# Performance work log

Measured on AMD Instinct MI355X. Metric: run time of the kernel, lower is better.

The kernel has to match this reference:

```python
import jax, jax.numpy as jnp
import numpy as np

N_U = 20000; N_I = 20000; D = 256
NNZ = 600000; EGG = 300000; EDD = 300000; B = 8192
DROP = 0.1; LAM2 = 1e-7


def _attention(x, W, a, edges):
    # GAT-style attention over sampled relationship edges (src -> tgt).
    n, d = x.shape
    h = x @ W                                  # [n, d]
    src, tgt = edges[0], edges[1]
    e = jax.nn.leaky_relu((h @ a[:d])[src] + (h @ a[d:])[tgt], 0.2)  # [E]
    m = jax.ops.segment_max(e, tgt, num_segments=n)
    m = jnp.where(jnp.isfinite(m), m, 0.0)
    ex = jnp.exp(e - m[tgt])
    denom = jax.ops.segment_sum(ex, tgt, num_segments=n)             # [n]
    num = jax.ops.segment_sum(ex[:, None] * h[src], tgt, num_segments=n)  # [n, d]
    return num / (denom[:, None] + 1e-9)


def _spmm(rows, cols, vals, x, n_out):
    # sparse [n_out, n_in] @ dense [n_in, d]
    return jax.ops.segment_sum(vals[:, None] * x[cols], rows, num_segments=n_out)


def _mlp(x, W1, b1, W2, b2, W3, b3):
    h = jax.nn.relu(x @ W1 + b1)
    h = jax.nn.relu(h @ W2 + b2)
    return (h @ W3 + b3)[..., 0]


def setup_inputs() -> dict:
    key = jax.random.key(0)
    ks = jax.random.split(key, 24)
    s = 0.02
    inp = {
        'E_g_0': jax.random.normal(ks[0], (N_U, D), jnp.float32) * s,
        'E_d_0': jax.random.normal(ks[1], (N_I, D), jnp.float32) * s,
        'att_W': jax.random.normal(ks[2], (D, D), jnp.float32) * s,
        'att_a': jax.random.normal(ks[3], (2 * D,), jnp.float32) * s,
        'att1_W': jax.random.normal(ks[4], (D, D), jnp.float32) * s,
        'att1_a': jax.random.normal(ks[5], (2 * D,), jnp.float32) * s,
        'W1': jax.random.normal(ks[6], (2 * D, D), jnp.float32) * s,
        'b1': jnp.zeros((D,), jnp.float32),
        'W2': jax.random.normal(ks[7], (D, D), jnp.float32) * s,
        'b2': jnp.zeros((D,), jnp.float32),
        'W3': jax.random.normal(ks[8], (D, 1), jnp.float32) * s,
        'b3': jnp.zeros((1,), jnp.float32),
        'M1': jax.random.normal(ks[9], (2 * D, D), jnp.float32) * s,
        'mb1': jnp.zeros((D,), jnp.float32),
        'M2': jax.random.normal(ks[10], (D, D), jnp.float32) * s,
        'mb2': jnp.zeros((D,), jnp.float32),
        'adj_vals': jax.random.uniform(ks[11], (NNZ,), jnp.float32),
        'uids': jax.random.randint(ks[12], (B,), 0, N_U, jnp.int32),
        'iids': jax.random.randint(ks[13], (B,), 0, N_I, jnp.int32),
        'pos': jax.random.randint(ks[14], (B,), 0, N_I, jnp.int32),
        'neg': jax.random.randint(ks[15], (B,), 0, N_I, jnp.int32),
        'gene_edges': jax.random.randint(ks[16], (2, EGG), 0, N_U, jnp.int32),
        'drug_edges': jax.random.randint(ks[17], (2, EDD), 0, N_I, jnp.int32),
        'adj_rows': jax.random.randint(ks[18], (NNZ,), 0, N_U, jnp.int32),
        'adj_cols': jax.random.randint(ks[19], (NNZ,), 0, N_I, jnp.int32),
        'drop1': jax.random.bernoulli(ks[20], 1.0 - DROP, (NNZ,)),
        'drop2': jax.random.bernoulli(ks[21], 1.0 - DROP, (NNZ,)),
    }
    return inp


def reference(E_g_0, E_d_0, att_W, att_a, att1_W, att1_a, W1, b1, W2, b2, W3, b3,
              M1, mb1, M2, mb2, adj_vals, uids, iids, pos, neg,
              gene_edges, drug_edges, adj_rows, adj_cols, drop1, drop2):
    # Attention-modulated layer-0 embeddings
    E_d0 = 0.1 * _attention(E_d_0, att_W, att_a, drug_edges) + E_d_0
    E_g0 = 0.1 * _attention(E_g_0, att_W, att_a, gene_edges) + E_g_0

    # sparse_dropout + spmm (two independent dropout draws, as in the source)
    scale = 1.0 / (1.0 - DROP)
    v1 = adj_vals * drop1.astype(adj_vals.dtype) * scale
    v2 = adj_vals * drop2.astype(adj_vals.dtype) * scale
    E_g = _spmm(adj_rows, adj_cols, v1, E_d0, N_U)   # adj @ E_d0
    E_d = _spmm(adj_cols, adj_rows, v2, E_g0, N_I)   # adj.T @ E_g0

    u = E_g[uids]; p = E_d[pos]; ng = E_d[neg]
    pos_s = _mlp(jnp.concatenate([u, p], axis=-1), W1, b1, W2, b2, W3, b3)
    neg_s = _mlp(jnp.concatenate([u, ng], axis=-1), W1, b1, W2, b2, W3, b3)

    # BCE-with-logits (labels 1 for pos, 0 for neg) + BPR term
    loss_pos = jnp.mean(jax.nn.softplus(-pos_s))
    loss_neg = jnp.mean(jax.nn.softplus(neg_s))
    loss_bpr = jnp.mean(jax.nn.softplus(-(pos_s - neg_s)))
    loss_r = loss_pos + loss_neg + loss_bpr

    params = (E_g_0, E_d_0, att_W, att_a, att1_W, att1_a,
              W1, b1, W2, b2, W3, b3, M1, mb1, M2, mb2)
    loss_reg = LAM2 * sum(jnp.sum(p_ * p_) for p_ in params)

    loss = loss_reg + loss_r  # loss_s == 0
    return jnp.stack([loss, loss_r, jnp.zeros((), loss.dtype)])
```

## Files before the change

### kernel.cpp

```cpp
#include <hip/hip_runtime.h>
#include <math.h>

#define N_NODES 20000
#define D       256
#define NNZ     600000
#define NEDGE   300000
#define BATCH   8192
#define DROP_SCALE (1.0f/0.9f)
#define LAM2_F  1e-7f

#define M_PAD   20096
#define CSTRIDE 20032

#define C_ATT 56
#define C_ADJ 80

#define BINW 320
#define NBIN 63
#define TILE_E 2048
#define EPT 8
#define T_ATT ((NEDGE + TILE_E - 1) / TILE_E)
#define T_ADJ ((NNZ + TILE_E - 1) / TILE_E)
#define NBLK_P1 (2 * T_ATT + 2 * T_ADJ)
#define CAP_BIN_ATT 5376
#define CAP_BIN_ADJ 6144

#define FP8_SCALE 256.0f
#define VSCALE    58980.0f
#define INV_VSCALE (1.0f/58980.0f)

typedef unsigned short u16;
typedef unsigned char  u8;
typedef __attribute__((ext_vector_type(8))) short bf16x8;
typedef __attribute__((ext_vector_type(4))) float f32x4;
typedef __attribute__((ext_vector_type(2))) float f32x2;
typedef __attribute__((ext_vector_type(4))) u16   v4h;
typedef __attribute__((ext_vector_type(4))) unsigned v4u;

__device__ inline float wave_reduce(float v) {
    #pragma unroll
    for (int off = 32; off > 0; off >>= 1) v += __shfl_down(v, off, 64);
    return v;
}

__device__ inline float softplus_f(float x) {
    float r = log1pf(__expf(-fabsf(x)));
    return x > 0.f ? x + r : r;
}

__device__ inline u16 f2bf(float f) {
    unsigned u = __float_as_uint(f);
    unsigned r = u + 0x7fff + ((u >> 16) & 1);
    return (u16)(r >> 16);
}
__device__ inline float bf2f(u16 b) { return __uint_as_float(((unsigned)b) << 16); }

__device__ inline u16 f2h(float f) {
    _Float16 h = (_Float16)f;
    return __builtin_bit_cast(u16, h);
}
__device__ inline float h2f(u16 b) {
    return (float)__builtin_bit_cast(_Float16, b);
}

__device__ inline unsigned f32x4_to_fp8x4(float a, float b, float c, float d) {
    int r = 0;
    r = __builtin_amdgcn_cvt_pk_fp8_f32(a, b, r, false);
    r = __builtin_amdgcn_cvt_pk_fp8_f32(c, d, r, true);
    return (unsigned)r;
}
__device__ inline u8 f32_to_fp8(float a) {
    int r = __builtin_amdgcn_cvt_pk_fp8_f32(a, a, 0, false);
    return (u8)(r & 0xff);
}

__device__ inline void gld_lds16(const void* g, void* l) {
    __builtin_amdgcn_global_load_lds((const __attribute__((address_space(1))) void*)g,
                                     (__attribute__((address_space(3))) void*)l, 16, 0, 0);
}

__global__ __launch_bounds__(256) void init_kernel(const unsigned char* __restrict__ drop,
                                                   const int* __restrict__ uids, const int* __restrict__ pos,
                                                   const int* __restrict__ neg,
                                                   const float* __restrict__ att_W, const float* __restrict__ att_a,
                                                   float* __restrict__ wlv, float* __restrict__ wrv,
                                                   unsigned* __restrict__ bm2, unsigned* __restrict__ bm3,
                                                   unsigned int* __restrict__ flag) {
    if (blockIdx.x < 96) {
        int i = blockIdx.x * blockDim.x + threadIdx.x;
        if (i < BATCH) {
            int v = uids[i];
            atomicOr(&bm2[v >> 5], 1u << (v & 31));
        } else if (i < 2 * BATCH) {
            int v = pos[i - BATCH];
            atomicOr(&bm3[v >> 5], 1u << (v & 31));
        } else {
            int v = neg[i - 2 * BATCH];
            atomicOr(&bm3[v >> 5], 1u << (v & 31));
        }
    } else if (blockIdx.x == 96) {
        __shared__ int cnt_s;
        if (threadIdx.x == 0) cnt_s = 0;
        __syncthreads();
        int c = 0;
        for (int i = threadIdx.x; i < 1024; i += blockDim.x)
            if (drop[4*i + 1] != 0) c++;
        atomicAdd(&cnt_s, c);
        __syncthreads();
        if (threadIdx.x == 0) *flag = (cnt_s > 64) ? 1u : 0u;
    } else {
        int t = threadIdx.x;
        float s1 = 0.f, s2 = 0.f;
        for (int n = 0; n < D; n++) {
            float w = att_W[(size_t)t * D + n];
            s1 += w * att_a[n];
            s2 += w * att_a[D + n];
        }
        wlv[t] = s1; wrv[t] = s2;
    }
}

#define NB_CAST (2 * M_PAD / 4)
#define NB_T1   (D * D / 256)
#define NB_T2   (2 * D * D / 256)
#define NB_T3   (D * D / 256)
#define NB_PREP (NB_CAST + NB_T1 + NB_T2 + NB_T3)
__global__ __launch_bounds__(256) void p1prep_kernel(
        const int* __restrict__ dtgt, const int* __restrict__ dsrc,
        const int* __restrict__ gtgt, const int* __restrict__ gsrc,
        const int* __restrict__ ar,   const int* __restrict__ ac,
        const float* __restrict__ vals,
        const void* __restrict__ drop1, const void* __restrict__ drop2,
        const unsigned int* __restrict__ flag,
        const unsigned* __restrict__ bm2, const unsigned* __restrict__ bm3,
        int* __restrict__ pcur, unsigned* __restrict__ attbin, uint2* __restrict__ adjbin,
        const float* __restrict__ E_g, const float* __restrict__ E_d,
        u16* __restrict__ Eg_bf, u16* __restrict__ Ed_bf,
        const float* __restrict__ att_W,
        const float* __restrict__ W1, const float* __restrict__ W2,
        u16* __restrict__ attWT, u16* __restrict__ W1T, u16* __restrict__ W2T,
        const float* __restrict__ wlv, const float* __restrict__ wrv,
        float* __restrict__ hl_g, float* __restrict__ hr_g,
        float* __restrict__ hl_d, float* __restrict__ hr_d,
        float* __restrict__ regp) {
    if (blockIdx.x < NBLK_P1) {
        __shared__ int hist[NBIN];
        __shared__ int basep[NBIN];
        for (int i = threadIdx.x; i < NBIN; i += 256) hist[i] = 0;
        __syncthreads();

        int b = blockIdx.x;
        int s, t0;
        if (b < T_ATT)               { s = 0; t0 = b; }
        else if (b < 2 * T_ATT)      { s = 1; t0 = b - T_ATT; }
        else if (b < 2*T_ATT + T_ADJ){ s = 2; t0 = b - 2 * T_ATT; }
        else                         { s = 3; t0 = b - 2 * T_ATT - T_ADJ; }
        int base = t0 * TILE_E;
        int regN = (s < 2) ? NEDGE : NNZ;

        int bins[EPT], rank[EPT];
        unsigned key[EPT], pay[EPT];
        float pv[EPT];

        if (s < 2) {
            const int* tgt = (s == 0) ? dtgt : gtgt;
            const int* src = (s == 0) ? dsrc : gsrc;
            #pragma unroll
            for (int e = 0; e < EPT; e++) {
                int idx = base + e * 256 + threadIdx.x;
                rank[e] = -1;
                if (idx < regN) {
                    int k = __builtin_nontemporal_load(tgt + idx);
                    int sv = __builtin_nontemporal_load(src + idx);
                    key[e] = (unsigned)k; pay[e] = (unsigned)sv;
                    bins[e] = k / BINW;
                    rank[e] = atomicAdd(&hist[bins[e]], 1);
                }
            }
        } else {
            const unsigned int bf = *flag;
            const int* keyp = (s == 2) ? ar : ac;
            const int* othp = (s == 2) ? ac : ar;
            const void* drp = (s == 2) ? drop1 : drop2;
            const unsigned* bm = (s == 2) ? bm2 : bm3;
            #pragma unroll
            for (int e = 0; e < EPT; e++) {
                int idx = base + e * 256 + threadIdx.x;
                rank[e] = -1;
                if (idx < regN) {
                    int k = __builtin_nontemporal_load(keyp + idx);
                    if ((bm[k >> 5] >> (k & 31)) & 1) {
                        bool keep = bf ? (__builtin_nontemporal_load((const u8*)drp + idx) != 0)
                                       : (__builtin_nontemporal_load((const unsigned*)drp + idx) != 0);
                        if (keep) {
                            float v = __builtin_nontemporal_load(vals + idx) * DROP_SCALE;
                            int oth = __builtin_nontemporal_load(othp + idx);
                            key[e] = (unsigned)k; pay[e] = (unsigned)oth; pv[e] = v;
                            bins[e] = k / BINW;
                            rank[e] = atomicAdd(&hist[bins[e]], 1);
                        }
                    }
                }
            }
        }
        __syncthreads();
        for (int i = threadIdx.x; i < NBIN; i += 256) {
            int h = hist[i];
            basep[i] = h ? atomicAdd(&pcur[s * NBIN + i], h) : 0;
        }
        __syncthreads();
        if (s < 2) {
            unsigned* seg = attbin + (size_t)s * NBIN * CAP_BIN_ATT;
            #pragma unroll
            for (int e = 0; e < EPT; e++) {
                if (rank[e] < 0) continue;
                int pos = basep[bins[e]] + rank[e];
                if (pos < CAP_BIN_ATT)
                    seg[(size_t)bins[e] * CAP_BIN_ATT + pos] = key[e] | (pay[e] << 16);
            }
        } else {
            uint2* seg = adjbin + (size_t)(s - 2) * NBIN * CAP_BIN_ADJ;
            #pragma unroll
            for (int e = 0; e < EPT; e++) {
                if (rank[e] < 0) continue;
                int pos = basep[bins[e]] + rank[e];
                if (pos < CAP_BIN_ADJ) {
                    uint2 pr; pr.x = key[e] | (pay[e] << 16); pr.y = __float_as_uint(pv[e]);
                    seg[(size_t)bins[e] * CAP_BIN_ADJ + pos] = pr;
                }
            }
        }
    } else {
        int bid = blockIdx.x - NBLK_P1;
        if (bid < NB_CAST) {
            int wid  = (bid * 256 + threadIdx.x) >> 6;
            int lane = threadIdx.x & 63;
            int is_d = (wid >= M_PAD);
            int row  = is_d ? wid - M_PAD : wid;
            u16* dst = (is_d ? Ed_bf : Eg_bf) + (size_t)row * D;
            float s3 = 0.f;
            if (row >= N_NODES) {
                ((ushort4*)dst)[lane] = make_ushort4(0, 0, 0, 0);
            } else {
                const float* src = (is_d ? E_d : E_g) + (size_t)row * D;
                float4 e  = ((const float4*)src)[lane];
                float4 l4 = ((const float4*)wlv)[lane];
                float4 r4 = ((const float4*)wrv)[lane];
                ((ushort4*)dst)[lane] = make_ushort4(f2bf(e.x), f2bf(e.y), f2bf(e.z), f2bf(e.w));
                float s1 = e.x*l4.x + e.y*l4.y + e.z*l4.z + e.w*l4.w;
                float s2 = e.x*r4.x + e.y*r4.y + e.z*r4.z + e.w*r4.w;
                s3 = e.x*e.x + e.y*e.y + e.z*e.z + e.w*e.w;
                s1 = wave_reduce(s1); s2 = wave_reduce(s2);
                if (lane == 0) {
                    if (is_d) { hl_d[row] = s1; hr_d[row] = s2; }
                    else      { hl_g[row] = s1; hr_g[row] = s2; }
                }
            }
            s3 = wave_reduce(s3);
            __shared__ float sm3[4];
            if (lane == 0) sm3[threadIdx.x >> 6] = s3;
            __syncthreads();
            if (threadIdx.x == 0) regp[bid] = sm3[0] + sm3[1] + sm3[2] + sm3[3];
        } else if (bid < NB_CAST + NB_T1) {
            int o = (bid - NB_CAST) * 256 + threadIdx.x;
            int n = o >> 8, k = o & 255;
            attWT[o] = f2bf(att_W[(size_t)k * D + n]);
        } else if (bid < NB_CAST + NB_T1 + NB_T2) {
            int o = (bid - NB_CAST - NB_T1) * 256 + threadIdx.x;
            int n = o / (2 * D), k = o - n * (2 * D);
            W1T[o] = f2bf(W1[(size_t)k * D + n]);
        } else {
            int o = (bid - NB_CAST - NB_T1 - NB_T2) * 256 + threadIdx.x;
            int n = o >> 8, k = o & 255;
            W2T[o] = f2bf(W2[(size_t)k * D + n]);
        }
    }
}

__global__ __launch_bounds__(1024) void p2_kernel(
        const int* __restrict__ pcur, const unsigned* __restrict__ attbin,
        const uint2* __restrict__ adjbin,
        const float* __restrict__ hl_d, const float* __restrict__ hr_d,
        const float* __restrict__ hl_g, const float* __restrict__ hr_g,
        int* __restrict__ cnt, unsigned* __restrict__ srcs, unsigned* __restrict__ adj) {
    int s   = blockIdx.x / NBIN;
    int bin = blockIdx.x - s * NBIN;
    int nodeBase = bin * BINW;
    __shared__ int cur[BINW];
    for (int t = threadIdx.x; t < BINW; t += blockDim.x) cur[t] = 0;
    __syncthreads();
    if (s < 2) {
        int m = pcur[s * NBIN + bin]; if (m > CAP_BIN_ATT) m = CAP_BIN_ATT;
        const unsigned* seg = attbin + ((size_t)s * NBIN + bin) * CAP_BIN_ATT;
        const float* hl = (s == 0) ? hl_d : hl_g;
        const float* hr = (s == 0) ? hr_d : hr_g;
        for (int k = threadIdx.x; k < m; k += blockDim.x) {
            unsigned e = seg[k];
            int lk  = (int)(e & 0xFFFFu) - nodeBase;
            int src = (int)(e >> 16);
            float ev = hl[src] + hr[nodeBase + lk];
            ev = ev > 0.f ? ev : 0.2f * ev;
            u16 xh = f2h(__expf(ev));
            int c = atomicAdd(&cur[lk], 1);
            if (c < C_ATT)
                srcs[(size_t)s * N_NODES * C_ATT + (size_t)(nodeBase + lk) * C_ATT + c] =
                    (unsigned)src | ((unsigned)xh << 16);
        }
        __syncthreads();
        for (int t = threadIdx.x; t < BINW; t += blockDim.x) {
            int node = nodeBase + t;
            if (node < N_NODES) {
                int n = cur[t]; if (n > C_ATT) n = C_ATT;
                cnt[s * CSTRIDE + node] = n;
            }
        }
    } else {
        int m = pcur[s * NBIN + bin]; if (m > CAP_BIN_ADJ) m = CAP_BIN_ADJ;
        const uint2* seg = adjbin + ((size_t)(s - 2) * NBIN + bin) * CAP_BIN_ADJ;
        for (int k = threadIdx.x; k < m; k += blockDim.x) {
            uint2 e = seg[k];
            int lk  = (int)(e.x & 0xFFFFu) - nodeBase;
            int oth = (int)(e.x >> 16);
            float v = __uint_as_float(e.y);
            unsigned pk = ((unsigned)(v * VSCALE + 0.5f) << 16) | (unsigned)oth;
            int c = atomicAdd(&cur[lk], 1);
            if (c < C_ADJ)
                adj[(size_t)(s - 2) * N_NODES * C_ADJ + (size_t)(nodeBase + lk) * C_ADJ + c] = pk;
        }
        __syncthreads();
        for (int t = threadIdx.x; t < BINW; t += blockDim.x) {
            int node = nodeBase + t;
            if (node < N_NODES) {
                int n = cur[t]; if (n > C_ADJ) n = C_ADJ;
                cnt[s * CSTRIDE + node] = n;
            }
        }
    }
}

__global__ __launch_bounds__(256) void gemm_bf16(const u16* __restrict__ A_, const u16* __restrict__ BT,
                                                 void* __restrict__ C_, int M, int N, int K,
                                                 const float* __restrict__ bias, int do_relu, int out_mode,
                                                 const u16* __restrict__ A2, void* __restrict__ C2,
                                                 const float* __restrict__ w3) {
    const u16* A = A_; void* C = C_;
    if (A2 && blockIdx.z == 1) { A = A2; C = C2; }
    __shared__ __align__(16) short As[128][32];
    __shared__ __align__(16) short Bs[128][32];
    int tid = threadIdx.x;
    int wave = tid >> 6, lane = tid & 63;
    int bm = blockIdx.x * 128, bn = blockIdx.y * 128;
    int sr = lane >> 2;
    int sc = (lane & 3) * 8;

    f32x4 acc[4][4];
    #pragma unroll
    for (int i = 0; i < 4; i++)
        #pragma unroll
        for (int j = 0; j < 4; j++)
            #pragma unroll
            for (int r = 0; r < 4; r++) acc[i][j][r] = 0.f;

    int wr = (wave >> 1) * 64;
    int wc = (wave & 1) * 64;
    int fr = lane & 15;
    int fk = (lane >> 4) * 8;

    for (int k0 = 0; k0 < K; k0 += 32) {
        #pragma unroll
        for (int j = 0; j < 2; j++) {
            int r0 = wave * 32 + j * 16;
            gld_lds16(A  + (size_t)(bm + r0 + sr) * K + k0 + sc, &As[r0][0]);
            gld_lds16(BT + (size_t)(bn + r0 + sr) * K + k0 + sc, &Bs[r0][0]);
        }
        __syncthreads();
        bf16x8 af[4], bfr[4];
        #pragma unroll
        for (int i = 0; i < 4; i++) af[i]  = *(const bf16x8*)&As[wr + i*16 + fr][fk];
        #pragma unroll
        for (int j = 0; j < 4; j++) bfr[j] = *(const bf16x8*)&Bs[wc + j*16 + fr][fk];
        #pragma unroll
        for (int i = 0; i < 4; i++)
            #pragma unroll
            for (int j = 0; j < 4; j++)
                acc[i][j] = __builtin_amdgcn_mfma_f32_16x16x32_bf16(af[i], bfr[j], acc[i][j], 0, 0, 0);
        __syncthreads();
    }

    if (out_mode == 2) {
        __shared__ float sacc[128];
        for (int t = tid; t < 128; t += 256) sacc[t] = 0.f;
        __syncthreads();
        float bvj[4], w3j[4];
        #pragma unroll
        for (int j = 0; j < 4; j++) {
            int col = bn + wc + j * 16 + fr;
            bvj[j] = bias[col];
            w3j[j] = w3[col];
        }
        #pragma unroll
        for (int i = 0; i < 4; i++) {
            #pragma unroll
            for (int r = 0; r < 4; r++) {
                float rs = 0.f;
                #pragma unroll
                for (int j = 0; j < 4; j++) {
                    float v = fmaxf(acc[i][j][r] + bvj[j], 0.f);
                    rs += v * w3j[j];
                }
                rs += __shfl_xor(rs, 1, 64);
                rs += __shfl_xor(rs, 2, 64);
                rs += __shfl_xor(rs, 4, 64);
                rs += __shfl_xor(rs, 8, 64);
                if (fr == 0)
                    atomicAdd(&sacc[wr + i * 16 + (lane >> 4) * 4 + r], rs);
            }
        }
        __syncthreads();
        float* sb = (float*)C;
        for (int t = tid; t < 128; t += 256)
            atomicAdd(&sb[bm + t], sacc[t]);
        return;
    }

    #pragma unroll
    for (int j = 0; j < 4; j++) {
        int col = bn + wc + j * 16 + fr;
        float bv = (bias && out_mode == 0) ? bias[col] : 0.f;
        #pragma unroll
        for (int i = 0; i < 4; i++) {
            #pragma unroll
            for (int r = 0; r < 4; r++) {
                int row = bm + wr + i * 16 + (lane >> 4) * 4 + r;
                if (row < M) {
                    float v = acc[i][j][r] + bv;
                    if (out_mode == 0) {
                        if (do_relu) v = fmaxf(v, 0.f);
                        ((u16*)C)[(size_t)row * N + col] = f2bf(v);
                    } else {
                        ((u8*)C)[(size_t)row * N + col] = f32_to_fp8(v * FP8_SCALE);
                    }
                }
            }
        }
    }
}

__global__ __launch_bounds__(256) void att_kernel(const u8* __restrict__ h_d, const u8* __restrict__ h_g,
                                                  const int* __restrict__ cur, const unsigned* __restrict__ srcs,
                                                  const u16* __restrict__ Ed_bf, const u16* __restrict__ Eg_bf,
                                                  u8* __restrict__ E_d0p, u8* __restrict__ E_g0p) {
    int wid  = (blockIdx.x * blockDim.x + threadIdx.x) >> 6;
    int lane = threadIdx.x & 63;
    if (wid >= 2 * N_NODES) return;
    int is_g = (wid >= N_NODES);
    int node = is_g ? wid - N_NODES : wid;
    const unsigned* h32 = (const unsigned*)(is_g ? h_g : h_d);
    int reg = is_g ? 1 : 0;
    const unsigned* sv = srcs + (size_t)reg * N_NODES * C_ATT + (size_t)node * C_ATT;
    int n = cur[reg * CSTRIDE + node];
    if (n > C_ATT) n = C_ATT;
    float ax = 0.f, ay = 0.f, az = 0.f, aw = 0.f, denom = 0.f;
    int k = 0;
    for (; k + 8 <= n; k += 8) {
        v4u qa = __builtin_nontemporal_load((const v4u*)(sv + k));
        v4u qb = __builtin_nontemporal_load((const v4u*)(sv + k + 4));
        unsigned g[8]; float x[8];
        #pragma unroll
        for (int j = 0; j < 4; j++) {
            g[j]     = h32[((size_t)(qa[j] & 0xFFFFu) << 6) + lane];
            g[4 + j] = h32[((size_t)(qb[j] & 0xFFFFu) << 6) + lane];
            x[j]     = h2f((u16)(qa[j] >> 16));
            x[4 + j] = h2f((u16)(qb[j] >> 16));
        }
        #pragma unroll
        for (int j = 0; j < 8; j++) {
            denom += x[j];
            f32x2 lo = __builtin_amdgcn_cvt_pk_f32_fp8(g[j], false);
            f32x2 hi = __builtin_amdgcn_cvt_pk_f32_fp8(g[j], true);
            ax += x[j]*lo[0]; ay += x[j]*lo[1]; az += x[j]*hi[0]; aw += x[j]*hi[1];
        }
    }
    for (; k + 4 <= n; k += 4) {
        v4u qa = __builtin_nontemporal_load((const v4u*)(sv + k));
        unsigned g[4]; float x[4];
        #pragma unroll
        for (int j = 0; j < 4; j++) {
            g[j] = h32[((size_t)(qa[j] & 0xFFFFu) << 6) + lane];
            x[j] = h2f((u16)(qa[j] >> 16));
        }
        #pragma unroll
        for (int j = 0; j < 4; j++) {
            denom += x[j];
            f32x2 lo = __builtin_amdgcn_cvt_pk_f32_fp8(g[j], false);
            f32x2 hi = __builtin_amdgcn_cvt_pk_f32_fp8(g[j], true);
            ax += x[j]*lo[0]; ay += x[j]*lo[1]; az += x[j]*hi[0]; aw += x[j]*hi[1];
        }
    }
    for (; k < n; k++) {
        unsigned q = sv[k];
        float xv = h2f((u16)(q >> 16));
        unsigned g = h32[((size_t)(q & 0xFFFFu) << 6) + lane];
        denom += xv;
        f32x2 lo = __builtin_amdgcn_cvt_pk_f32_fp8(g, false);
        f32x2 hi = __builtin_amdgcn_cvt_pk_f32_fp8(g, true);
        ax += xv*lo[0]; ay += xv*lo[1]; az += xv*hi[0]; aw += xv*hi[1];
    }
    float sc = 0.1f / (denom + 1e-9f);
    const u16* E0b = is_g ? Eg_bf : Ed_bf;
    u8*       out  = is_g ? E_g0p : E_d0p;
    ushort4 b4 = ((const ushort4*)(E0b + (size_t)node * D))[lane];
    unsigned pk = f32x4_to_fp8x4(FP8_SCALE * bf2f(b4.x) + sc * ax, FP8_SCALE * bf2f(b4.y) + sc * ay,
                                 FP8_SCALE * bf2f(b4.z) + sc * az, FP8_SCALE * bf2f(b4.w) + sc * aw);
    ((unsigned*)(out + (size_t)node * D))[lane] = pk;
}

__global__ __launch_bounds__(256) void pull_kernel(const int* __restrict__ uids, const int* __restrict__ pos,
                                                   const int* __restrict__ neg,
                                                   const int* __restrict__ cur, const unsigned* __restrict__ adj,
                                                   const u8* __restrict__ E_d0p, const u8* __restrict__ E_g0p,
                                                   u16* __restrict__ X) {
    int wid  = (blockIdx.x * blockDim.x + threadIdx.x) >> 6;
    int lane = threadIdx.x & 63;
    if (wid >= 3 * BATCH) return;
    int type = wid >> 13;
    int b    = wid & (BATCH - 1);
    int node, reg; const u8* E;
    if (type == 0)      { node = uids[b]; reg = 2; E = E_d0p; }
    else if (type == 1) { node = pos[b];  reg = 3; E = E_g0p; }
    else                { node = neg[b];  reg = 3; E = E_g0p; }
    const unsigned* E32 = (const unsigned*)E;
    const unsigned* av = adj + (size_t)(reg - 2) * N_NODES * C_ADJ + (size_t)node * C_ADJ;
    int n = cur[reg * CSTRIDE + node];
    if (n > C_ADJ) n = C_ADJ;
    float ax = 0.f, ay = 0.f, az = 0.f, aw = 0.f;
    int k = 0;
    for (; k + 8 <= n; k += 8) {
        v4u qa = __builtin_nontemporal_load((const v4u*)(av + k));
        v4u qb = __builtin_nontemporal_load((const v4u*)(av + k + 4));
        unsigned g[8]; float v[8];
        #pragma unroll
        for (int j = 0; j < 4; j++) {
            g[j]     = E32[((size_t)(qa[j] & 0xFFFFu) << 6) + lane];
            g[4 + j] = E32[((size_t)(qb[j] & 0xFFFFu) << 6) + lane];
            v[j]     = (float)(qa[j] >> 16) * INV_VSCALE;
            v[4 + j] = (float)(qb[j] >> 16) * INV_VSCALE;
        }
        #pragma unroll
        for (int j = 0; j < 8; j++) {
            f32x2 lo = __builtin_amdgcn_cvt_pk_f32_fp8(g[j], false);
            f32x2 hi = __builtin_amdgcn_cvt_pk_f32_fp8(g[j], true);
            ax += v[j]*lo[0]; ay += v[j]*lo[1]; az += v[j]*hi[0]; aw += v[j]*hi[1];
        }
    }
    for (; k + 4 <= n; k += 4) {
        v4u qa = __builtin_nontemporal_load((const v4u*)(av + k));
        unsigned g[4]; float v[4];
        #pragma unroll
        for (int j = 0; j < 4; j++) {
            g[j] = E32[((size_t)(qa[j] & 0xFFFFu) << 6) + lane];
            v[j] = (float)(qa[j] >> 16) * INV_VSCALE;
        }
        #pragma unroll
        for (int j = 0; j < 4; j++) {
            f32x2 lo = __builtin_amdgcn_cvt_pk_f32_fp8(g[j], false);
            f32x2 hi = __builtin_amdgcn_cvt_pk_f32_fp8(g[j], true);
            ax += v[j]*lo[0]; ay += v[j]*lo[1]; az += v[j]*hi[0]; aw += v[j]*hi[1];
        }
    }
    for (; k < n; k++) {
        unsigned q = av[k];
        int c = q & 0xFFFF;
        float v = (float)(q >> 16) * INV_VSCALE;
        unsigned g = E32[((size_t)c << 6) + lane];
        f32x2 lo = __builtin_amdgcn_cvt_pk_f32_fp8(g, false);
        f32x2 hi = __builtin_amdgcn_cvt_pk_f32_fp8(g, true);
        ax += v*lo[0]; ay += v*lo[1]; az += v*hi[0]; aw += v*hi[1];
    }
    const float inv = 1.0f / FP8_SCALE;
    ushort4 r = make_ushort4(f2bf(ax * inv), f2bf(ay * inv), f2bf(az * inv), f2bf(aw * inv));
    if (type == 0) {
        ((ushort4*)(X + (size_t)b * 2 * D))[lane] = r;
        ((ushort4*)(X + (size_t)(BATCH + b) * 2 * D))[lane] = r;
    } else if (type == 1) {
        ((ushort4*)(X + (size_t)b * 2 * D + D))[lane] = r;
    } else {
        ((ushort4*)(X + (size_t)(BATCH + b) * 2 * D + D))[lane] = r;
    }
}

struct RegArgs { const float* p[14]; int n[14]; };
#define NB_REG  448
#define NB_LOSS 16
#define NB_TAIL (NB_REG + NB_LOSS)

__global__ __launch_bounds__(256) void tail_kernel(RegArgs ra, const float* __restrict__ s,
                                                   const float* __restrict__ b3p,
                                                   const float* __restrict__ regp,
                                                   float* __restrict__ acc, float* __restrict__ out) {
    int bid = blockIdx.x;
    int w = threadIdx.x >> 6, lane = threadIdx.x & 63;
    __shared__ float sm[3][4];
    __shared__ int lastf;
    if (bid < NB_REG) {
        const float* p = ra.p[bid >> 5];
        int n = ra.n[bid >> 5];
        int base = (bid & 31) * 4096;
        if (base < n) {
            float sum = 0.f;
            if (base + 4096 <= n) {
                const float4* p4 = (const float4*)(p + base);
                float4 v = p4[threadIdx.x];
                sum += v.x*v.x + v.y*v.y + v.z*v.z + v.w*v.w;
                v = p4[256 + threadIdx.x];
                sum += v.x*v.x + v.y*v.y + v.z*v.z + v.w*v.w;
                v = p4[512 + threadIdx.x];
                sum += v.x*v.x + v.y*v.y + v.z*v.z + v.w*v.w;
                v = p4[768 + threadIdx.x];
                sum += v.x*v.x + v.y*v.y + v.z*v.z + v.w*v.w;
            } else {
                for (int i = base + threadIdx.x; i < n; i += 256) { float v = p[i]; sum += v * v; }
            }
            sum = wave_reduce(sum);
            if (lane == 0) sm[0][w] = sum;
            __syncthreads();
            if (threadIdx.x == 0)
                atomicAdd(&acc[0], sm[0][0] + sm[0][1] + sm[0][2] + sm[0][3]);
        }
    } else {
        float b3 = b3p[0];
        float lp = 0.f, ln = 0.f, lb = 0.f;
        for (int i = (bid - NB_REG) * 256 + threadIdx.x; i < BATCH; i += NB_LOSS * 256) {
            float ps = s[i] + b3, ns = s[BATCH + i] + b3;
            lp += softplus_f(-ps);
            ln += softplus_f(ns);
            lb += softplus_f(-(ps - ns));
        }
        lp = wave_reduce(lp); ln = wave_reduce(ln); lb = wave_reduce(lb);
        if (lane == 0) { sm[0][w] = lp; sm[1][w] = ln; sm[2][w] = lb; }
        __syncthreads();
        if (threadIdx.x == 0) {
            float a = 0.f, b = 0.f, c = 0.f;
            for (int i = 0; i < 4; i++) { a += sm[0][i]; b += sm[1][i]; c += sm[2][i]; }
            atomicAdd(&acc[1], a); atomicAdd(&acc[2], b); atomicAdd(&acc[3], c);
        }
    }
    __syncthreads();
    if (threadIdx.x == 0) {
        __threadfence();
        unsigned t = atomicAdd((unsigned*)&acc[8], 1u);
        lastf = (t == NB_TAIL - 1);
    }
    __syncthreads();
    if (!lastf) return;
    float sum = 0.f;
    for (int i = threadIdx.x; i < NB_CAST; i += 256) sum += regp[i];
    sum = wave_reduce(sum);
    if (lane == 0) sm[0][w] = sum;
    __syncthreads();
    if (threadIdx.x == 0) {
        __threadfence();
        float a0 = atomicAdd(&acc[0], 0.f);
        float a1 = atomicAdd(&acc[1], 0.f);
        float a2 = atomicAdd(&acc[2], 0.f);
        float a3 = atomicAdd(&acc[3], 0.f);
        float reg = a0 + sm[0][0] + sm[0][1] + sm[0][2] + sm[0][3];
        float lr = (a1 + a2 + a3) * (1.0f / (float)BATCH);
        out[0] = LAM2_F * reg + lr;
        out[1] = lr;
        out[2] = 0.f;
    }
}

extern "C" void kernel_launch(void* const* d_in, const int* in_sizes, int n_in,
                              void* d_out, int out_size, void* d_ws, size_t ws_size,
                              hipStream_t stream) {
    (void)n_in; (void)out_size; (void)ws_size;
    const float* E_g_0   = (const float*)d_in[0];
    const float* E_d_0   = (const float*)d_in[1];
    const float* att_W   = (const float*)d_in[2];
    const float* att_a   = (const float*)d_in[3];
    const float* W1      = (const float*)d_in[6];
    const float* b1      = (const float*)d_in[7];
    const float* W2      = (const float*)d_in[8];
    const float* b2      = (const float*)d_in[9];
    const float* W3      = (const float*)d_in[10];
    const float* b3      = (const float*)d_in[11];
    const float* adj_vals= (const float*)d_in[16];
    const int*   uids    = (const int*)d_in[17];
    const int*   pos     = (const int*)d_in[19];
    const int*   neg     = (const int*)d_in[20];
    const int*   gene_e  = (const int*)d_in[21];
    const int*   drug_e  = (const int*)d_in[22];
    const int*   adj_rows= (const int*)d_in[23];
    const int*   adj_cols= (const int*)d_in[24];
    const void*  drop1   = d_in[25];
    const void*  drop2   = d_in[26];

    char* ws = (char*)d_ws;
    size_t cur_off = 0;
    auto take = [&](size_t bytes) -> void* {
        void* p = ws + cur_off;
        cur_off += (bytes + 255) & ~(size_t)255;
        return p;
    };
    u16* Eg_bf = (u16*)take((size_t)M_PAD * D * 2);
    u16* Ed_bf = (u16*)take((size_t)M_PAD * D * 2);
    u16* X     = Eg_bf;
    u16* attWT = (u16*)take((size_t)D * D * 2);
    u16* W1T   = (u16*)take((size_t)D * 2 * D * 2);
    u16* W2T   = (u16*)take((size_t)D * D * 2);
    u8*  h_g   = (u8*)take((size_t)M_PAD * D);
    u8*  h_d   = (u8*)take((size_t)M_PAD * D);
    u8*  E_g0p = (u8*)take((size_t)N_NODES * D);
    u8*  E_d0p = (u8*)take((size_t)N_NODES * D);
    u16* H1    = (u16*)take((size_t)2 * BATCH * D * 2);
    float* hl_g = (float*)take((size_t)N_NODES * 4);
    float* hr_g = (float*)take((size_t)N_NODES * 4);
    float* hl_d = (float*)take((size_t)N_NODES * 4);
    float* hr_d = (float*)take((size_t)N_NODES * 4);
    float* wlv  = (float*)take((size_t)D * 4);
    float* wrv  = (float*)take((size_t)D * 4);
    float* regp = (float*)take((size_t)NB_CAST * 4);
    unsigned* srcs = (unsigned*)take((size_t)2 * N_NODES * C_ATT * 4);
    unsigned* adj  = (unsigned*)take((size_t)2 * N_NODES * C_ADJ * 4);
    int*   cnt  = (int*)take((size_t)4 * CSTRIDE * 4);
    unsigned* attbin = (unsigned*)take((size_t)2 * NBIN * CAP_BIN_ATT * 4);
    uint2*    adjbin = (uint2*)take((size_t)2 * NBIN * CAP_BIN_ADJ * 8);
    int*      pcur = (int*)take((size_t)4 * NBIN * 4);
    unsigned* bm2  = (unsigned*)take(4096);
    unsigned* bm3  = (unsigned*)take(4096);
    float*    acc  = (float*)take(256);
    float*    sbuf = (float*)take((size_t)2 * BATCH * 4);
    size_t zbytes = (char*)sbuf + (size_t)2 * BATCH * 4 - (char*)pcur;

    hipMemsetAsync(pcur, 0, zbytes, stream);
    init_kernel<<<98, 256, 0, stream>>>((const unsigned char*)drop1, uids, pos, neg,
                                        att_W, att_a, wlv, wrv,
                                        bm2, bm3, (unsigned int*)(acc + 4));

    p1prep_kernel<<<NBLK_P1 + NB_PREP, 256, 0, stream>>>(
        drug_e + NEDGE, drug_e, gene_e + NEDGE, gene_e,
        adj_rows, adj_cols, adj_vals, drop1, drop2,
        (const unsigned int*)(acc + 4), bm2, bm3,
        pcur, attbin, adjbin,
        E_g_0, E_d_0, Eg_bf, Ed_bf, att_W, W1, W2,
        attWT, W1T, W2T, wlv, wrv, hl_g, hr_g, hl_d, hr_d, regp);

    p2_kernel<<<4 * NBIN, 1024, 0, stream>>>(pcur, attbin, adjbin,
                                             hl_d, hr_d, hl_g, hr_g, cnt, srcs, adj);

    gemm_bf16<<<dim3(M_PAD / 128, 2, 2), 256, 0, stream>>>(Eg_bf, attWT, h_g, N_NODES, D, D,
                                                           nullptr, 0, 1, Ed_bf, h_d, nullptr);
    att_kernel<<<10000, 256, 0, stream>>>(h_d, h_g, cnt, srcs,
                                          Ed_bf, Eg_bf, E_d0p, E_g0p);

    pull_kernel<<<6144, 256, 0, stream>>>(uids, pos, neg, cnt, adj, E_d0p, E_g0p, X);

    gemm_bf16<<<dim3(2 * BATCH / 128, 2, 1), 256, 0, stream>>>(X,  W1T, H1, 2 * BATCH, D, 2 * D,
                                                               b1, 1, 0, nullptr, nullptr, nullptr);
    gemm_bf16<<<dim3(2 * BATCH / 128, 2, 1), 256, 0, stream>>>(H1, W2T, sbuf, 2 * BATCH, D, D,
                                                               b2, 1, 2, nullptr, nullptr, W3);

    RegArgs ra;
    for (int i = 0; i < 14; i++) { ra.p[i] = (const float*)d_in[i + 2]; ra.n[i] = in_sizes[i + 2]; }
    tail_kernel<<<NB_TAIL, 256, 0, stream>>>(ra, sbuf, b3, regp, acc, (float*)d_out);
}
```

Baseline: 326.5 us.

## Merge small kernels: fold reg loss into prep, p2 with attention GEMM, loss into last GEMM

Moves the parameter L2-regularization reduction into extra blocks of the prep kernel. Merges the bucketing pass (p2, now at 256 threads) and the attention feature GEMM into one launch, since they are independent. Folds the final BCE/BPR loss reduction into the last MLP GEMM using a last-block ticket. This cuts two kernel launches and the serialization gaps between them, but the last GEMM block now does a serial single-block reduction and p2 runs with fewer threads per block.

```diff
diff --git a/kernel.cpp b/kernel.cpp
--- a/kernel.cpp
+++ b/kernel.cpp
@@ -34,7 +34,6 @@
 typedef __attribute__((ext_vector_type(8))) short bf16x8;
 typedef __attribute__((ext_vector_type(4))) float f32x4;
 typedef __attribute__((ext_vector_type(2))) float f32x2;
-typedef __attribute__((ext_vector_type(4))) u16   v4h;
 typedef __attribute__((ext_vector_type(4))) unsigned v4u;
 
 __device__ inline float wave_reduce(float v) {
@@ -78,6 +77,8 @@
     __builtin_amdgcn_global_load_lds((const __attribute__((address_space(1))) void*)g,
                                      (__attribute__((address_space(3))) void*)l, 16, 0, 0);
 }
+
+struct RegArgs { const float* p[14]; int n[14]; };
 
 __global__ __launch_bounds__(256) void init_kernel(const unsigned char* __restrict__ drop,
                                                    const int* __restrict__ uids, const int* __restrict__ pos,
@@ -125,6 +126,7 @@
 #define NB_T2   (2 * D * D / 256)
 #define NB_T3   (D * D / 256)
 #define NB_PREP (NB_CAST + NB_T1 + NB_T2 + NB_T3)
+#define NB_REG  448
 __global__ __launch_bounds__(256) void p1prep_kernel(
         const int* __restrict__ dtgt, const int* __restrict__ dsrc,
         const int* __restrict__ gtgt, const int* __restrict__ gsrc,
@@ -142,7 +144,7 @@
         const float* __restrict__ wlv, const float* __restrict__ wrv,
         float* __restrict__ hl_g, float* __restrict__ hr_g,
         float* __restrict__ hl_d, float* __restrict__ hr_d,
-        float* __restrict__ regp) {
+        float* __restrict__ regp, RegArgs ra, float* __restrict__ acc) {
     if (blockIdx.x < NBLK_P1) {
         __shared__ int hist[NBIN];
         __shared__ int basep[NBIN];
@@ -232,9 +234,9 @@
         }
     } else {
         int bid = blockIdx.x - NBLK_P1;
+        int w = threadIdx.x >> 6, lane = threadIdx.x & 63;
         if (bid < NB_CAST) {
             int wid  = (bid * 256 + threadIdx.x) >> 6;
-            int lane = threadIdx.x & 63;
             int is_d = (wid >= M_PAD);
             int row  = is_d ? wid - M_PAD : wid;
             u16* dst = (is_d ? Ed_bf : Eg_bf) + (size_t)row * D;
@@ -269,82 +271,176 @@
             int o = (bid - NB_CAST - NB_T1) * 256 + threadIdx.x;
             int n = o / (2 * D), k = o - n * (2 * D);
             W1T[o] = f2bf(W1[(size_t)k * D + n]);
-        } else {
+        } else if (bid < NB_PREP) {
             int o = (bid - NB_CAST - NB_T1 - NB_T2) * 256 + threadIdx.x;
             int n = o >> 8, k = o & 255;
             W2T[o] = f2bf(W2[(size_t)k * D + n]);
-        }
-    }
-}
-
-__global__ __launch_bounds__(1024) void p2_kernel(
+        } else {
+            int rb = bid - NB_PREP;
+            const float* p = ra.p[rb >> 5];
+            int n = ra.n[rb >> 5];
+            int base = (rb & 31) * 4096;
+            if (base >= n) return;
+            float sum = 0.f;
+            if (base + 4096 <= n) {
+                const float4* p4 = (const float4*)(p + base);
+                float4 v = p4[threadIdx.x];
+                sum += v.x*v.x + v.y*v.y + v.z*v.z + v.w*v.w;
+                v = p4[256 + threadIdx.x];
+                sum += v.x*v.x + v.y*v.y + v.z*v.z + v.w*v.w;
+                v = p4[512 + threadIdx.x];
+                sum += v.x*v.x + v.y*v.y + v.z*v.z + v.w*v.w;
+                v = p4[768 + threadIdx.x];
+                sum += v.x*v.x + v.y*v.y + v.z*v.z + v.w*v.w;
+            } else {
+                for (int i = base + threadIdx.x; i < n; i += 256) { float v = p[i]; sum += v * v; }
+            }
+            sum = wave_reduce(sum);
+            __shared__ float smr[4];
+            if (lane == 0) smr[w] = sum;
+            __syncthreads();
+            if (threadIdx.x == 0)
+                atomicAdd(&acc[0], smr[0] + smr[1] + smr[2] + smr[3]);
+        }
+    }
+}
+
+#define NB_P2   (4 * NBIN)
+#define NB_ATTG ((M_PAD / 128) * 4)
+__global__ __launch_bounds__(256) void p2gemm_kernel(
         const int* __restrict__ pcur, const unsigned* __restrict__ attbin,
         const uint2* __restrict__ adjbin,
         const float* __restrict__ hl_d, const float* __restrict__ hr_d,
         const float* __restrict__ hl_g, const float* __restrict__ hr_g,
-        int* __restrict__ cnt, unsigned* __restrict__ srcs, unsigned* __restrict__ adj) {
-    int s   = blockIdx.x / NBIN;
-    int bin = blockIdx.x - s * NBIN;
-    int nodeBase = bin * BINW;
-    __shared__ int cur[BINW];
-    for (int t = threadIdx.x; t < BINW; t += blockDim.x) cur[t] = 0;
-    __syncthreads();
-    if (s < 2) {
-        int m = pcur[s * NBIN + bin]; if (m > CAP_BIN_ATT) m = CAP_BIN_ATT;
-        const unsigned* seg = attbin + ((size_t)s * NBIN + bin) * CAP_BIN_ATT;
-        const float* hl = (s == 0) ? hl_d : hl_g;
-        const float* hr = (s == 0) ? hr_d : hr_g;
-        for (int k = threadIdx.x; k < m; k += blockDim.x) {
-            unsigned e = seg[k];
-            int lk  = (int)(e & 0xFFFFu) - nodeBase;
-            int src = (int)(e >> 16);
-            float ev = hl[src] + hr[nodeBase + lk];
-            ev = ev > 0.f ? ev : 0.2f * ev;
-            u16 xh = f2h(__expf(ev));
-            int c = atomicAdd(&cur[lk], 1);
-            if (c < C_ATT)
-                srcs[(size_t)s * N_NODES * C_ATT + (size_t)(nodeBase + lk) * C_ATT + c] =
-                    (unsigned)src | ((unsigned)xh << 16);
-        }
-        __syncthreads();
-        for (int t = threadIdx.x; t < BINW; t += blockDim.x) {
-            int node = nodeBase + t;
-            if (node < N_NODES) {
-                int n = cur[t]; if (n > C_ATT) n = C_ATT;
-                cnt[s * CSTRIDE + node] = n;
+        int* __restrict__ cnt, unsigned* __restrict__ srcs, unsigned* __restrict__ adj,
+        const u16* __restrict__ Eg_bf, const u16* __restrict__ Ed_bf,
+        const u16* __restrict__ attWT, u8* __restrict__ h_g, u8* __restrict__ h_d) {
+    if (blockIdx.x < NB_P2) {
+        int s   = blockIdx.x / NBIN;
+        int bin = blockIdx.x - s * NBIN;
+        int nodeBase = bin * BINW;
+        __shared__ int cur[BINW];
+        for (int t = threadIdx.x; t < BINW; t += 256) cur[t] = 0;
+        __syncthreads();
+        if (s < 2) {
+            int m = pcur[s * NBIN + bin]; if (m > CAP_BIN_ATT) m = CAP_BIN_ATT;
+            const unsigned* seg = attbin + ((size_t)s * NBIN + bin) * CAP_BIN_ATT;
+            const float* hl = (s == 0) ? hl_d : hl_g;
+            const float* hr = (s == 0) ? hr_d : hr_g;
+            for (int k = threadIdx.x; k < m; k += 256) {
+                unsigned e = seg[k];
+                int lk  = (int)(e & 0xFFFFu) - nodeBase;
+                int src = (int)(e >> 16);
+                float ev = hl[src] + hr[nodeBase + lk];
+                ev = ev > 0.f ? ev : 0.2f * ev;
+                u16 xh = f2h(__expf(ev));
+                int c = atomicAdd(&cur[lk], 1);
+                if (c < C_ATT)
+                    srcs[(size_t)s * N_NODES * C_ATT + (size_t)(nodeBase + lk) * C_ATT + c] =
+                        (unsigned)src | ((unsigned)xh << 16);
+            }
+            __syncthreads();
+            for (int t = threadIdx.x; t < BINW; t += 256) {
+                int node = nodeBase + t;
+                if (node < N_NODES) {
+                    int n = cur[t]; if (n > C_ATT) n = C_ATT;
+                    cnt[s * CSTRIDE + node] = n;
+                }
+            }
+        } else {
+            int m = pcur[s * NBIN + bin]; if (m > CAP_BIN_ADJ) m = CAP_BIN_ADJ;
+            const uint2* seg = adjbin + ((size_t)(s - 2) * NBIN + bin) * CAP_BIN_ADJ;
+            for (int k = threadIdx.x; k < m; k += 256) {
+                uint2 e = seg[k];
+                int lk  = (int)(e.x & 0xFFFFu) - nodeBase;
+                int oth = (int)(e.x >> 16);
+                float v = __uint_as_float(e.y);
+                unsigned pk = ((unsigned)(v * VSCALE + 0.5f) << 16) | (unsigned)oth;
+                int c = atomicAdd(&cur[lk], 1);
+                if (c < C_ADJ)
+                    adj[(size_t)(s - 2) * N_NODES * C_ADJ + (size_t)(nodeBase + lk) * C_ADJ + c] = pk;
+            }
+            __syncthreads();
+            for (int t = threadIdx.x; t < BINW; t += 256) {
+                int node = nodeBase + t;
+                if (node < N_NODES) {
+                    int n = cur[t]; if (n > C_ADJ) n = C_ADJ;
+                    cnt[s * CSTRIDE + node] = n;
+                }
             }
         }
     } else {
-        int m = pcur[s * NBIN + bin]; if (m > CAP_BIN_ADJ) m = CAP_BIN_ADJ;
-        const uint2* seg = adjbin + ((size_t)(s - 2) * NBIN + bin) * CAP_BIN_ADJ;
-        for (int k = threadIdx.x; k < m; k += blockDim.x) {
-            uint2 e = seg[k];
-            int lk  = (int)(e.x & 0xFFFFu) - nodeBase;
-            int oth = (int)(e.x >> 16);
-            float v = __uint_as_float(e.y);
-            unsigned pk = ((unsigned)(v * VSCALE + 0.5f) << 16) | (unsigned)oth;
-            int c = atomicAdd(&cur[lk], 1);
-            if (c < C_ADJ)
-                adj[(size_t)(s - 2) * N_NODES * C_ADJ + (size_t)(nodeBase + lk) * C_ADJ + c] = pk;
-        }
-        __syncthreads();
-        for (int t = threadIdx.x; t < BINW; t += blockDim.x) {
-            int node = nodeBase + t;
-            if (node < N_NODES) {
-                int n = cur[t]; if (n > C_ADJ) n = C_ADJ;
-                cnt[s * CSTRIDE + node] = n;
-            }
-        }
-    }
-}
-
-__global__ __launch_bounds__(256) void gemm_bf16(const u16* __restrict__ A_, const u16* __restrict__ BT,
-                                                 void* __restrict__ C_, int M, int N, int K,
+        int t  = blockIdx.x - NB_P2;
+        int z  = t / (2 * (M_PAD / 128));
+        int r  = t - z * (2 * (M_PAD / 128));
+        int by = r / (M_PAD / 128);
+        int bx = r - by * (M_PAD / 128);
+        const u16* A = z ? Ed_bf : Eg_bf;
+        u8* C = z ? h_d : h_g;
+        __shared__ __align__(16) short As[128][32];
+        __shared__ __align__(16) short Bs[128][32];
+        int tid = threadIdx.x;
+        int wave = tid >> 6, lane = tid & 63;
+        int bm = bx * 128, bn = by * 128;
+        int sr = lane >> 2;
+        int sc = (lane & 3) * 8;
+
+        f32x4 acc[4][4];
+        #pragma unroll
+        for (int i = 0; i < 4; i++)
+            #pragma unroll
+            for (int j = 0; j < 4; j++)
+                #pragma unroll
+                for (int q = 0; q < 4; q++) acc[i][j][q] = 0.f;
+
+        int wr = (wave >> 1) * 64;
+        int wc = (wave & 1) * 64;
+        int fr = lane & 15;
+        int fk = (lane >> 4) * 8;
+
+        for (int k0 = 0; k0 < D; k0 += 32) {
+            #pragma unroll
+            for (int j = 0; j < 2; j++) {
+                int r0 = wave * 32 + j * 16;
+                gld_lds16(A     + (size_t)(bm + r0 + sr) * D + k0 + sc, &As[r0][0]);
+                gld_lds16(attWT + (size_t)(bn + r0 + sr) * D + k0 + sc, &Bs[r0][0]);
+            }
+            __syncthreads();
+            bf16x8 af[4], bfr[4];
+            #pragma unroll
+            for (int i = 0; i < 4; i++) af[i]  = *(const bf16x8*)&As[wr + i*16 + fr][fk];
+            #pragma unroll
+            for (int j = 0; j < 4; j++) bfr[j] = *(const bf16x8*)&Bs[wc + j*16 + fr][fk];
+            #pragma unroll
+            for (int i = 0; i < 4; i++)
+                #pragma unroll
+                for (int j = 0; j < 4; j++)
+                    acc[i][j] = __builtin_amdgcn_mfma_f32_16x16x32_bf16(af[i], bfr[j], acc[i][j], 0, 0, 0);
+            __syncthreads();
+        }
+
+        #pragma unroll
+        for (int j = 0; j < 4; j++) {
+            int col = bn + wc + j * 16 + fr;
+            #pragma unroll
+            for (int i = 0; i < 4; i++) {
+                #pragma unroll
+                for (int q = 0; q < 4; q++) {
+                    int row = bm + wr + i * 16 + (lane >> 4) * 4 + q;
+                    if (row < N_NODES)
+                        C[(size_t)row * D + col] = f32_to_fp8(acc[i][j][q] * FP8_SCALE);
+                }
+            }
+        }
+    }
+}
+
+__global__ __launch_bounds__(256) void gemm_bf16(const u16* __restrict__ A, const u16* __restrict__ BT,
+                                                 void* __restrict__ C, int M, int N, int K,
                                                  const float* __restrict__ bias, int do_relu, int out_mode,
-                                                 const u16* __restrict__ A2, void* __restrict__ C2,
-                                                 const float* __restrict__ w3) {
-    const u16* A = A_; void* C = C_;
-    if (A2 && blockIdx.z == 1) { A = A2; C = C2; }
+                                                 const float* __restrict__ w3,
+                                                 const float* __restrict__ b3p, const float* __restrict__ regp,
+                                                 float* __restrict__ accp, float* __restrict__ outp) {
     __shared__ __align__(16) short As[128][32];
     __shared__ __align__(16) short Bs[128][32];
     int tid = threadIdx.x;
@@ -420,13 +516,45 @@
         float* sb = (float*)C;
         for (int t = tid; t < 128; t += 256)
             atomicAdd(&sb[bm + t], sacc[t]);
+
+        __threadfence();
+        __shared__ unsigned tick;
+        if (tid == 0) tick = atomicAdd((unsigned*)&accp[8], 1u);
+        __syncthreads();
+        unsigned total = gridDim.x * gridDim.y * gridDim.z;
+        if (tick != total - 1) return;
+
+        float b3 = b3p[0];
+        float lp = 0.f, ln = 0.f, lb = 0.f;
+        for (int i = tid; i < BATCH; i += 256) {
+            float ps = __hip_atomic_load(&sb[i], __ATOMIC_RELAXED, __HIP_MEMORY_SCOPE_AGENT) + b3;
+            float ns = __hip_atomic_load(&sb[BATCH + i], __ATOMIC_RELAXED, __HIP_MEMORY_SCOPE_AGENT) + b3;
+            lp += softplus_f(-ps);
+            ln += softplus_f(ns);
+            lb += softplus_f(-(ps - ns));
+        }
+        float rsum = 0.f;
+        for (int i = tid; i < NB_CAST; i += 256) rsum += regp[i];
+        lp = wave_reduce(lp); ln = wave_reduce(ln); lb = wave_reduce(lb); rsum = wave_reduce(rsum);
+        __shared__ float smf[4][4];
+        if (lane == 0) { smf[0][wave] = lp; smf[1][wave] = ln; smf[2][wave] = lb; smf[3][wave] = rsum; }
+        __syncthreads();
+        if (tid == 0) {
+            float a = 0.f, b = 0.f, c = 0.f, rg = 0.f;
+            for (int i = 0; i < 4; i++) { a += smf[0][i]; b += smf[1][i]; c += smf[2][i]; rg += smf[3][i]; }
+            float reg0 = __hip_atomic_load(&accp[0], __ATOMIC_RELAXED, __HIP_MEMORY_SCOPE_AGENT);
+            float lr = (a + b + c) * (1.0f / (float)BATCH);
+            outp[0] = LAM2_F * (reg0 + rg) + lr;
+            outp[1] = lr;
+            outp[2] = 0.f;
+        }
         return;
     }
 
     #pragma unroll
     for (int j = 0; j < 4; j++) {
         int col = bn + wc + j * 16 + fr;
-        float bv = (bias && out_mode == 0) ? bias[col] : 0.f;
+        float bv = bias ? bias[col] : 0.f;
         #pragma unroll
         for (int i = 0; i < 4; i++) {
             #pragma unroll
@@ -434,12 +562,8 @@
                 int row = bm + wr + i * 16 + (lane >> 4) * 4 + r;
                 if (row < M) {
                     float v = acc[i][j][r] + bv;
-                    if (out_mode == 0) {
-                        if (do_relu) v = fmaxf(v, 0.f);
-                        ((u16*)C)[(size_t)row * N + col] = f2bf(v);
-                    } else {
-                        ((u8*)C)[(size_t)row * N + col] = f32_to_fp8(v * FP8_SCALE);
-                    }
+                    if (do_relu) v = fmaxf(v, 0.f);
+                    ((u16*)C)[(size_t)row * N + col] = f2bf(v);
                 }
             }
         }
@@ -586,89 +710,6 @@
         ((ushort4*)(X + (size_t)b * 2 * D + D))[lane] = r;
     } else {
         ((ushort4*)(X + (size_t)(BATCH + b) * 2 * D + D))[lane] = r;
-    }
-}
-
-struct RegArgs { const float* p[14]; int n[14]; };
-#define NB_REG  448
-#define NB_LOSS 16
-#define NB_TAIL (NB_REG + NB_LOSS)
-
-__global__ __launch_bounds__(256) void tail_kernel(RegArgs ra, const float* __restrict__ s,
-                                                   const float* __restrict__ b3p,
-                                                   const float* __restrict__ regp,
-                                                   float* __restrict__ acc, float* __restrict__ out) {
-    int bid = blockIdx.x;
-    int w = threadIdx.x >> 6, lane = threadIdx.x & 63;
-    __shared__ float sm[3][4];
-    __shared__ int lastf;
-    if (bid < NB_REG) {
-        const float* p = ra.p[bid >> 5];
-        int n = ra.n[bid >> 5];
-        int base = (bid & 31) * 4096;
-        if (base < n) {
-            float sum = 0.f;
-            if (base + 4096 <= n) {
-                const float4* p4 = (const float4*)(p + base);
-                float4 v = p4[threadIdx.x];
-                sum += v.x*v.x + v.y*v.y + v.z*v.z + v.w*v.w;
-                v = p4[256 + threadIdx.x];
-                sum += v.x*v.x + v.y*v.y + v.z*v.z + v.w*v.w;
-                v = p4[512 + threadIdx.x];
-                sum += v.x*v.x + v.y*v.y + v.z*v.z + v.w*v.w;
-                v = p4[768 + threadIdx.x];
-                sum += v.x*v.x + v.y*v.y + v.z*v.z + v.w*v.w;
-            } else {
-                for (int i = base + threadIdx.x; i < n; i += 256) { float v = p[i]; sum += v * v; }
-            }
-            sum = wave_reduce(sum);
-            if (lane == 0) sm[0][w] = sum;
-            __syncthreads();
-            if (threadIdx.x == 0)
-                atomicAdd(&acc[0], sm[0][0] + sm[0][1] + sm[0][2] + sm[0][3]);
-        }
-    } else {
-        float b3 = b3p[0];
-        float lp = 0.f, ln = 0.f, lb = 0.f;
-        for (int i = (bid - NB_REG) * 256 + threadIdx.x; i < BATCH; i += NB_LOSS * 256) {
-            float ps = s[i] + b3, ns = s[BATCH + i] + b3;
-            lp += softplus_f(-ps);
-            ln += softplus_f(ns);
-            lb += softplus_f(-(ps - ns));
-        }
-        lp = wave_reduce(lp); ln = wave_reduce(ln); lb = wave_reduce(lb);
-        if (lane == 0) { sm[0][w] = lp; sm[1][w] = ln; sm[2][w] = lb; }
-        __syncthreads();
-        if (threadIdx.x == 0) {
-            float a = 0.f, b = 0.f, c = 0.f;
-            for (int i = 0; i < 4; i++) { a += sm[0][i]; b += sm[1][i]; c += sm[2][i]; }
-            atomicAdd(&acc[1], a); atomicAdd(&acc[2], b); atomicAdd(&acc[3], c);
-        }
-    }
-    __syncthreads();
-    if (threadIdx.x == 0) {
-        __threadfence();
-        unsigned t = atomicAdd((unsigned*)&acc[8], 1u);
-        lastf = (t == NB_TAIL - 1);
-    }
-    __syncthreads();
-    if (!lastf) return;
-    float sum = 0.f;
-    for (int i = threadIdx.x; i < NB_CAST; i += 256) sum += regp[i];
-    sum = wave_reduce(sum);
-    if (lane == 0) sm[0][w] = sum;
-    __syncthreads();
-    if (threadIdx.x == 0) {
-        __threadfence();
-        float a0 = atomicAdd(&acc[0], 0.f);
-        float a1 = atomicAdd(&acc[1], 0.f);
-        float a2 = atomicAdd(&acc[2], 0.f);
-        float a3 = atomicAdd(&acc[3], 0.f);
-        float reg = a0 + sm[0][0] + sm[0][1] + sm[0][2] + sm[0][3];
-        float lr = (a1 + a2 + a3) * (1.0f / (float)BATCH);
-        out[0] = LAM2_F * reg + lr;
-        out[1] = lr;
-        out[2] = 0.f;
     }
 }
 
@@ -739,30 +780,29 @@
                                         att_W, att_a, wlv, wrv,
                                         bm2, bm3, (unsigned int*)(acc + 4));
 
-    p1prep_kernel<<<NBLK_P1 + NB_PREP, 256, 0, stream>>>(
+    RegArgs ra;
+    for (int i = 0; i < 14; i++) { ra.p[i] = (const float*)d_in[i + 2]; ra.n[i] = in_sizes[i + 2]; }
+    p1prep_kernel<<<NBLK_P1 + NB_PREP + NB_REG, 256, 0, stream>>>(
         drug_e + NEDGE, drug_e, gene_e + NEDGE, gene_e,
         adj_rows, adj_cols, adj_vals, drop1, drop2,
         (const unsigned int*)(acc + 4), bm2, bm3,
         pcur, attbin, adjbin,
         E_g_0, E_d_0, Eg_bf, Ed_bf, att_W, W1, W2,
-        attWT, W1T, W2T, wlv, wrv, hl_g, hr_g, hl_d, hr_d, regp);
-
-    p2_kernel<<<4 * NBIN, 1024, 0, stream>>>(pcur, attbin, adjbin,
-                                             hl_d, hr_d, hl_g, hr_g, cnt, srcs, adj);
-
-    gemm_bf16<<<dim3(M_PAD / 128, 2, 2), 256, 0, stream>>>(Eg_bf, attWT, h_g, N_NODES, D, D,
-                                                           nullptr, 0, 1, Ed_bf, h_d, nullptr);
+        attWT, W1T, W2T, wlv, wrv, hl_g, hr_g, hl_d, hr_d, regp, ra, acc);
+
+    p2gemm_kernel<<<NB_P2 + NB_ATTG, 256, 0, stream>>>(
+        pcur, attbin, adjbin, hl_d, hr_d, hl_g, hr_g, cnt, srcs, adj,
+        Eg_bf, Ed_bf, attWT, h_g, h_d);
+
     att_kernel<<<10000, 256, 0, stream>>>(h_d, h_g, cnt, srcs,
                                           Ed_bf, Eg_bf, E_d0p, E_g0p);
 
     pull_kernel<<<6144, 256, 0, stream>>>(uids, pos, neg, cnt, adj, E_d0p, E_g0p, X);
 
-    gemm_bf16<<<dim3(2 * BATCH / 128, 2, 1), 256, 0, stream>>>(X,  W1T, H1, 2 * BATCH, D, 2 * D,
-                                                               b1, 1, 0, nullptr, nullptr, nullptr);
-    gemm_bf16<<<dim3(2 * BATCH / 128, 2, 1), 256, 0, stream>>>(H1, W2T, sbuf, 2 * BATCH, D, D,
-                                                               b2, 1, 2, nullptr, nullptr, W3);
-
-    RegArgs ra;
-    for (int i = 0; i < 14; i++) { ra.p[i] = (const float*)d_in[i + 2]; ra.n[i] = in_sizes[i + 2]; }
-    tail_kernel<<<NB_TAIL, 256, 0, stream>>>(ra, sbuf, b3, regp, acc, (float*)d_out);
-}
+    gemm_bf16<<<dim3(2 * BATCH / 128, 2, 1), 256, 0, stream>>>(
+        X, W1T, H1, 2 * BATCH, D, 2 * D, b1, 1, 0,
+        nullptr, nullptr, nullptr, nullptr, nullptr);
+    gemm_bf16<<<dim3(2 * BATCH / 128, 2, 1), 256, 0, stream>>>(
+        H1, W2T, sbuf, 2 * BATCH, D, D, b2, 1, 2,
+        W3, b3, regp, acc, (float*)d_out);
+}
```

Result: slower. 337.9 us (+3.5%).
